# Optimization experiments

Measured on AMD Instinct MI355X. Metric: run time of the kernel, lower is better.

Reference implementation:

```python
import jax, jax.numpy as jnp
import numpy as np

N_NODES = 50000
N_EDGES = 800000
IN_CH = 128
HID = 64
PROJ = 32


def _gcn_norm(edge_index, n):
    # add self loops, symmetric normalization D^-1/2 (A+I) D^-1/2
    loop = jnp.arange(n, dtype=edge_index.dtype)
    src = jnp.concatenate([edge_index[0], loop])
    dst = jnp.concatenate([edge_index[1], loop])
    deg = jax.ops.segment_sum(jnp.ones_like(dst, jnp.float32), dst, num_segments=n)
    dinv = deg ** -0.5  # deg >= 1 due to self loops
    norm = dinv[src] * dinv[dst]
    return src, dst, norm


def _propagate(h, src, dst, norm, n):
    # gather -> scale -> scatter-add (message passing along A_hat)
    return jax.ops.segment_sum(h[src] * norm[:, None], dst, num_segments=n)


def _ho_gcn_layer(x, src, dst, norm, Ws, b, n):
    # out = sum_{k=1..max_order} (A_hat^k x) W_k + b
    out = jnp.zeros((n, Ws[0].shape[1]), x.dtype)
    h = x
    for W in Ws:
        h = _propagate(h, src, dst, norm, n)
        out = out + h @ W
    return out + b


def setup_inputs() -> dict:
    key = jax.random.key(0)
    ks = jax.random.split(key, 16)

    def w(k, fan_in, fan_out):
        return (jax.random.normal(k, (fan_in, fan_out), jnp.float32) / np.sqrt(fan_in)).astype(jnp.float32)

    x = jax.random.normal(ks[0], (N_NODES, IN_CH), jnp.float32)
    edge_index = jax.random.randint(ks[1], (2, N_EDGES), 0, N_NODES, dtype=jnp.int64)
    return {
        "x": x,
        "edge_index": edge_index,
        # conv1: max_order=2 -> two weights
        "W1_1": w(ks[2], IN_CH, HID), "W1_2": w(ks[3], IN_CH, HID),
        "b1": jnp.zeros((HID,), jnp.float32),
        # conv2
        "W2_1": w(ks[4], HID, HID // 2), "W2_2": w(ks[5], HID, HID // 2),
        "b2": jnp.zeros((HID // 2,), jnp.float32),
        # projection head
        "Wp1": w(ks[6], HID // 2, PROJ), "bp1": jnp.zeros((PROJ,), jnp.float32),
        "Wp2": w(ks[7], PROJ, PROJ), "bp2": jnp.zeros((PROJ,), jnp.float32),
        # coordinate head
        "Wc1": w(ks[8], HID // 2, HID // 4), "bc1": jnp.zeros((HID // 4,), jnp.float32),
        "Wc2": w(ks[9], HID // 4, 2), "bc2": jnp.zeros((2,), jnp.float32),
    }


def reference(x, edge_index, W1_1, W1_2, b1, W2_1, W2_2, b2,
              Wp1, bp1, Wp2, bp2, Wc1, bc1, Wc2, bc2):
    n = x.shape[0]
    src, dst, norm = _gcn_norm(edge_index, n)
    h1 = jax.nn.relu(_ho_gcn_layer(x, src, dst, norm, (W1_1, W1_2), b1, n))
    # dropout is identity in eval/reference mode
    h2 = jax.nn.relu(_ho_gcn_layer(h1, src, dst, norm, (W2_1, W2_2), b2, n))
    z = jax.nn.relu(h2 @ Wp1 + bp1) @ Wp2 + bp2
    coordinates = jax.nn.relu(h2 @ Wc1 + bc1) @ Wc2 + bc2
    return (coordinates, z)
```

## Files before the change

kernel.cpp:

```cpp
#include <hip/hip_runtime.h>

#define NN 50000
#define NE 800000
#define S 4
#define BINW 12500
#define NN4 (NN * S)
#define NBLK2 ((NN4 + 255) / 256)
#define NBG ((NN + 63) / 64)
#define NBH ((NE + 255) / 256)

__global__ __launch_bounds__(256) void zero_cnt_k(int* __restrict__ cnt) {
    int i = blockIdx.x * blockDim.x + threadIdx.x;
    if (i < NN4) cnt[i] = 0;
}

__global__ __launch_bounds__(256) void gemm1_hist_k(const float* __restrict__ A,
                                                    const float* __restrict__ WA,
                                                    const float* __restrict__ WB,
                                                    float* __restrict__ outA,
                                                    float* __restrict__ outB,
                                                    const int* __restrict__ src,
                                                    const int* __restrict__ dst,
                                                    int* __restrict__ cnt,
                                                    int* __restrict__ rank) {
    if (blockIdx.x >= NBG) {
        int e = (blockIdx.x - NBG) * 256 + threadIdx.x;
        if (e < NE) {
            int s = src[e], d = dst[e];
            int b = s / BINW;
            rank[e] = atomicAdd(&cnt[d * S + b], 1);
        }
        return;
    }

    __shared__ float As[64 * 36];
    __shared__ float W1s[32 * 68];
    __shared__ float W2s[32 * 68];
    const int t = threadIdx.x;
    const int tj = t & 15;
    const int tn = t >> 4;
    const int n0 = blockIdx.x * 64;
    float acc[4][8] = {};

    for (int kc = 0; kc < 128; kc += 32) {
        if (kc) __syncthreads();
        {
            int idx = t;
#pragma unroll
            for (int r = 0; r < 2; r++, idx += 256) {
                int nl = idx >> 3, q = idx & 7;
                int node = n0 + nl; node = node < NN ? node : NN - 1;
                float4 a = ((const float4*)A)[(size_t)node * 32 + (kc >> 2) + q];
                *(float4*)&As[nl * 36 + q * 4] = a;
            }
        }
        {
            int idx = t;
#pragma unroll
            for (int r = 0; r < 2; r++, idx += 256) {
                int kl = idx >> 4, j4 = idx & 15;
                *(float4*)&W1s[kl * 68 + j4 * 4] = ((const float4*)WA)[(size_t)(kc + kl) * 16 + j4];
                *(float4*)&W2s[kl * 68 + j4 * 4] = ((const float4*)WB)[(size_t)(kc + kl) * 16 + j4];
            }
        }
        __syncthreads();

        const float* ap = &As[tn * 4 * 36];
        const float* w1p = &W1s[tj * 4];
        const float* w2p = &W2s[tj * 4];
#pragma unroll 2
        for (int k4 = 0; k4 < 8; k4++) {
            float4 a0 = *(const float4*)&ap[0 * 36 + k4 * 4];
            float4 a1 = *(const float4*)&ap[1 * 36 + k4 * 4];
            float4 a2 = *(const float4*)&ap[2 * 36 + k4 * 4];
            float4 a3 = *(const float4*)&ap[3 * 36 + k4 * 4];
#pragma unroll
            for (int kk = 0; kk < 4; kk++) {
                float4 w1 = *(const float4*)&w1p[(k4 * 4 + kk) * 68];
                float4 w2 = *(const float4*)&w2p[(k4 * 4 + kk) * 68];
                float av0 = kk == 0 ? a0.x : kk == 1 ? a0.y : kk == 2 ? a0.z : a0.w;
                float av1 = kk == 0 ? a1.x : kk == 1 ? a1.y : kk == 2 ? a1.z : a1.w;
                float av2 = kk == 0 ? a2.x : kk == 1 ? a2.y : kk == 2 ? a2.z : a2.w;
                float av3 = kk == 0 ? a3.x : kk == 1 ? a3.y : kk == 2 ? a3.z : a3.w;
#define FMA8(m, AV)                                                     \
                acc[m][0] += AV * w1.x; acc[m][1] += AV * w1.y;          \
                acc[m][2] += AV * w1.z; acc[m][3] += AV * w1.w;          \
                acc[m][4] += AV * w2.x; acc[m][5] += AV * w2.y;          \
                acc[m][6] += AV * w2.z; acc[m][7] += AV * w2.w;
                FMA8(0, av0)
                FMA8(1, av1)
                FMA8(2, av2)
                FMA8(3, av3)
#undef FMA8
            }
        }
    }

#pragma unroll
    for (int m = 0; m < 4; m++) {
        int node = n0 + tn * 4 + m;
        if (node < NN) {
            *(float4*)&outA[(size_t)node * 64 + tj * 4] =
                make_float4(acc[m][0], acc[m][1], acc[m][2], acc[m][3]);
            *(float4*)&outB[(size_t)node * 64 + tj * 4] =
                make_float4(acc[m][4], acc[m][5], acc[m][6], acc[m][7]);
        }
    }
}

__global__ __launch_bounds__(256) void sum_blocks_k(const int* __restrict__ cnt,
                                                    int* __restrict__ bsum,
                                                    float* __restrict__ dinv) {
    __shared__ int s[256];
    int t = threadIdx.x;
    int i = blockIdx.x * 256 + t;
    int v = (i < NN4) ? cnt[i] : 0;
    s[t] = v;
    if (i < NN4 && (i & 3) == 0) {
        int deg = cnt[i] + cnt[i + 1] + cnt[i + 2] + cnt[i + 3];
        dinv[i >> 2] = rsqrtf((float)(deg + 1));
    }
    __syncthreads();
    for (int off = 128; off > 0; off >>= 1) {
        if (t < off) s[t] += s[t + off];
        __syncthreads();
    }
    if (t == 0) bsum[blockIdx.x] = s[0];
}

__global__ __launch_bounds__(256) void scan_final_k(const int* __restrict__ cnt,
                                                    const int* __restrict__ bsum,
                                                    int* __restrict__ rowsS) {
    __shared__ int sOff[256];
    __shared__ int s[256];
    int t = threadIdx.x;
    int accum = 0;
    for (int idx = t; idx < NBLK2; idx += 256)
        if (idx < blockIdx.x) accum += bsum[idx];
    sOff[t] = accum;
    __syncthreads();
    for (int off = 128; off > 0; off >>= 1) {
        if (t < off) sOff[t] += sOff[t + off];
        __syncthreads();
    }
    int boff = sOff[0];

    int i = blockIdx.x * 256 + t;
    int v = (i < NN4) ? cnt[i] : 0;
    s[t] = v;
    __syncthreads();
    for (int off = 1; off < 256; off <<= 1) {
        int x = (t >= off) ? s[t - off] : 0;
        __syncthreads();
        s[t] += x;
        __syncthreads();
    }
    if (i < NN4) rowsS[i] = boff + s[t] - v;
    if (blockIdx.x == 0 && t == 0) rowsS[NN4] = NE;
}

__global__ __launch_bounds__(256) void scatter_k(const int* __restrict__ src,
                                                 const int* __restrict__ dst,
                                                 const int* __restrict__ rank,
                                                 const int* __restrict__ rowsS,
                                                 int* __restrict__ col) {
    int e = blockIdx.x * blockDim.x + threadIdx.x;
    if (e >= NE) return;
    int s = src[e], d = dst[e];
    int b = s / BINW;
    col[rowsS[d * S + b] + rank[e]] = s;
}

template<int LOG2C4, bool ADDIN>
__global__ __launch_bounds__(256) void prop_k(const float4* __restrict__ h4,
                                              const float4* __restrict__ addin4,
                                              const float* __restrict__ bias,
                                              float4* __restrict__ out4,
                                              const int* __restrict__ rowsS,
                                              const int* __restrict__ col,
                                              const float* __restrict__ dinv) {
    const int C4 = 1 << LOG2C4;
    unsigned tid = blockIdx.x * blockDim.x + threadIdx.x;
    unsigned node = tid >> LOG2C4;
    if (node >= NN) return;
    unsigned lane = tid & (C4 - 1);
    size_t rowoff = ((size_t)node << LOG2C4) + lane;
    float dn = dinv[node];
    float w0 = dn * dn;
    float4 hv = h4[rowoff];
    float4 acc;
    if (ADDIN) {
        float4 a = addin4[rowoff];
        acc.x = a.x + w0 * hv.x; acc.y = a.y + w0 * hv.y;
        acc.z = a.z + w0 * hv.z; acc.w = a.w + w0 * hv.w;
    } else {
        float4 b = ((const float4*)bias)[lane];
        acc.x = b.x + w0 * hv.x; acc.y = b.y + w0 * hv.y;
        acc.z = b.z + w0 * hv.z; acc.w = b.w + w0 * hv.w;
    }
    int base = node * S;
    int rs = rowsS[base];
#pragma unroll
    for (int p = 1; p <= S; p++) {
        int re = rowsS[base + p];
        int i = rs;
        for (; i + 4 <= re; i += 4) {
            int c0 = col[i + 0];
            int c1 = col[i + 1];
            int c2 = col[i + 2];
            int c3 = col[i + 3];
            float4 v0 = h4[((size_t)c0 << LOG2C4) + lane];
            float4 v1 = h4[((size_t)c1 << LOG2C4) + lane];
            float4 v2 = h4[((size_t)c2 << LOG2C4) + lane];
            float4 v3 = h4[((size_t)c3 << LOG2C4) + lane];
            float a0 = dinv[c0] * dn;
            float a1 = dinv[c1] * dn;
            float a2 = dinv[c2] * dn;
            float a3 = dinv[c3] * dn;
            acc.x += a0 * v0.x + a1 * v1.x + a2 * v2.x + a3 * v3.x;
            acc.y += a0 * v0.y + a1 * v1.y + a2 * v2.y + a3 * v3.y;
            acc.z += a0 * v0.z + a1 * v1.z + a2 * v2.z + a3 * v3.z;
            acc.w += a0 * v0.w + a1 * v1.w + a2 * v2.w + a3 * v3.w;
        }
        for (; i < re; i++) {
            int c = col[i];
            float4 v = h4[((size_t)c << LOG2C4) + lane];
            float w = dinv[c] * dn;
            acc.x += w * v.x; acc.y += w * v.y; acc.z += w * v.z; acc.w += w * v.w;
        }
        rs = re;
    }
    if (!ADDIN) {
        acc.x = fmaxf(acc.x, 0.0f); acc.y = fmaxf(acc.y, 0.0f);
        acc.z = fmaxf(acc.z, 0.0f); acc.w = fmaxf(acc.w, 0.0f);
    }
    out4[rowoff] = acc;
}

template<int K, int JW>
__global__ __launch_bounds__(256) void gemm_k(const float* __restrict__ A,
                                              const float* __restrict__ WA,
                                              const float* __restrict__ WB,
                                              float* __restrict__ out, int n) {
    __shared__ float As[64 * 68];
    __shared__ float Ws[64 * 68];
    const int t = threadIdx.x;
    const int tj = t & 15;
    const int tn = t >> 4;
    const int n0 = blockIdx.x * 64;
    float acc[4][4] = {};

    for (int kc = 0; kc < K; kc += 64) {
        if (kc) __syncthreads();
        {
            int idx = t;
#pragma unroll
            for (int r = 0; r < 4; r++, idx += 256) {
                int nl = idx >> 4, q = idx & 15;
                int node = n0 + nl; node = node < n ? node : n - 1;
                float4 a = ((const float4*)A)[(size_t)node * (K / 4) + (kc >> 2) + q];
                *(float4*)&As[nl * 68 + q * 4] = a;
            }
        }
        {
            int idx = t;
#pragma unroll
            for (int r = 0; r < 4; r++, idx += 256) {
                int kl = idx >> 4, j4 = idx & 15;
                const float* W = (j4 < 8) ? WA : WB;
                float4 w = ((const float4*)W)[(size_t)(kc + kl) * 8 + (j4 & 7)];
                *(float4*)&Ws[kl * 68 + j4 * 4] = w;
            }
        }
        __syncthreads();

        const float* ap = &As[tn * 4 * 68];
        const float* wp = &Ws[tj * 4];
#pragma unroll 4
        for (int k4 = 0; k4 < 16; k4++) {
            float4 a0 = *(const float4*)&ap[0 * 68 + k4 * 4];
            float4 a1 = *(const float4*)&ap[1 * 68 + k4 * 4];
            float4 a2 = *(const float4*)&ap[2 * 68 + k4 * 4];
            float4 a3 = *(const float4*)&ap[3 * 68 + k4 * 4];
            float4 w0 = *(const float4*)&wp[(k4 * 4 + 0) * 68];
            float4 w1 = *(const float4*)&wp[(k4 * 4 + 1) * 68];
            float4 w2 = *(const float4*)&wp[(k4 * 4 + 2) * 68];
            float4 w3 = *(const float4*)&wp[(k4 * 4 + 3) * 68];
#define FMA_ROW(m, AV)                                                   \
            acc[m][0] += AV.x * w0.x + AV.y * w1.x + AV.z * w2.x + AV.w * w3.x; \
            acc[m][1] += AV.x * w0.y + AV.y * w1.y + AV.z * w2.y + AV.w * w3.y; \
            acc[m][2] += AV.x * w0.z + AV.y * w1.z + AV.z * w2.z + AV.w * w3.z; \
            acc[m][3] += AV.x * w0.w + AV.y * w1.w + AV.z * w2.w + AV.w * w3.w;
            FMA_ROW(0, a0)
            FMA_ROW(1, a1)
            FMA_ROW(2, a2)
            FMA_ROW(3, a3)
#undef FMA_ROW
        }
    }

    int mat = tj >> 3;
    int jw = (tj & 7) * 4;
    float* ob = out + (size_t)mat * n * JW + jw;
#pragma unroll
    for (int m = 0; m < 4; m++) {
        int node = n0 + tn * 4 + m;
        if (node < n)
            *(float4*)&ob[(size_t)node * JW] =
                make_float4(acc[m][0], acc[m][1], acc[m][2], acc[m][3]);
    }
}

__global__ __launch_bounds__(256) void heads_k(const float* __restrict__ h2,
                                               const float* __restrict__ Wp1, const float* __restrict__ bp1,
                                               const float* __restrict__ Wp2, const float* __restrict__ bp2,
                                               const float* __restrict__ Wc1, const float* __restrict__ bc1,
                                               const float* __restrict__ Wc2, const float* __restrict__ bc2,
                                               float* __restrict__ coord, float* __restrict__ z, int n) {
    __shared__ float sWp1[32 * 32], sWp2[32 * 32], sWc1[32 * 16], sWc2[32];
    __shared__ float sbp1[32], sbp2[32], sbc1[16], sbc2[2];
    __shared__ float sh[32 * 36], st[32 * 36], stc[32 * 18];
    const int t = threadIdx.x;
    for (int i = t; i < 1024; i += 256) { sWp1[i] = Wp1[i]; sWp2[i] = Wp2[i]; }
    for (int i = t; i < 512; i += 256) sWc1[i] = Wc1[i];
    if (t < 32) { sWc2[t] = Wc2[t]; sbp1[t] = bp1[t]; sbp2[t] = bp2[t]; }
    if (t < 16) sbc1[t] = bc1[t];
    if (t < 2) sbc2[t] = bc2[t];

    const int n0 = blockIdx.x * 32;
    const int nl = t >> 3;
    const int jq = t & 7;
    const int node = n0 + nl;
    {
        float4 v = make_float4(0.f, 0.f, 0.f, 0.f);
        if (node < n) v = *(const float4*)&h2[(size_t)node * 32 + jq * 4];
        *(float4*)&sh[nl * 36 + jq * 4] = v;
    }
    __syncthreads();

    float4 a = *(const float4*)&sbp1[jq * 4];
#pragma unroll
    for (int k = 0; k < 32; k++) {
        float hv = sh[nl * 36 + k];
        float4 w = *(const float4*)&sWp1[k * 32 + jq * 4];
        a.x += hv * w.x; a.y += hv * w.y; a.z += hv * w.z; a.w += hv * w.w;
    }
    a.x = fmaxf(a.x, 0.f); a.y = fmaxf(a.y, 0.f);
    a.z = fmaxf(a.z, 0.f); a.w = fmaxf(a.w, 0.f);
    *(float4*)&st[nl * 36 + jq * 4] = a;

    float2 c = *(const float2*)&sbc1[jq * 2];
#pragma unroll
    for (int k = 0; k < 32; k++) {
        float hv = sh[nl * 36 + k];
        float2 w = *(const float2*)&sWc1[k * 16 + jq * 2];
        c.x += hv * w.x; c.y += hv * w.y;
    }
    c.x = fmaxf(c.x, 0.f); c.y = fmaxf(c.y, 0.f);
    *(float2*)&stc[nl * 18 + jq * 2] = c;
    __syncthreads();

    float4 zz = *(const float4*)&sbp2[jq * 4];
#pragma unroll
    for (int k = 0; k < 32; k++) {
        float tv = st[nl * 36 + k];
        float4 w = *(const float4*)&sWp2[k * 32 + jq * 4];
        zz.x += tv * w.x; zz.y += tv * w.y; zz.z += tv * w.z; zz.w += tv * w.w;
    }
    if (node < n) *(float4*)&z[(size_t)node * 32 + jq * 4] = zz;

    if (jq < 2) {
        float s = sbc2[jq];
#pragma unroll
        for (int k = 0; k < 16; k++) s += stc[nl * 18 + k] * sWc2[k * 2 + jq];
        if (node < n) coord[(size_t)node * 2 + jq] = s;
    }
}

extern "C" void kernel_launch(void* const* d_in, const int* in_sizes, int n_in,
                              void* d_out, int out_size, void* d_ws, size_t ws_size,
                              hipStream_t stream) {
    const float* x    = (const float*)d_in[0];
    const int*   ei   = (const int*)d_in[1];
    const int*   src  = ei;
    const int*   dst  = ei + NE;
    const float* W1_1 = (const float*)d_in[2];
    const float* W1_2 = (const float*)d_in[3];
    const float* b1   = (const float*)d_in[4];
    const float* W2_1 = (const float*)d_in[5];
    const float* W2_2 = (const float*)d_in[6];
    const float* b2   = (const float*)d_in[7];
    const float* Wp1  = (const float*)d_in[8];
    const float* bp1  = (const float*)d_in[9];
    const float* Wp2  = (const float*)d_in[10];
    const float* bp2  = (const float*)d_in[11];
    const float* Wc1  = (const float*)d_in[12];
    const float* bc1  = (const float*)d_in[13];
    const float* Wc2  = (const float*)d_in[14];
    const float* bc2  = (const float*)d_in[15];

    float* ws    = (float*)d_ws;
    float* dinv  = ws;
    int*   cnt   = (int*)(dinv + NN);
    int*   rowsS = cnt + NN4;
    int*   bsum  = rowsS + NN4 + 4;
    int*   rank  = bsum + 1024;
    int*   col   = rank + NE;
    float* bufY  = (float*)(col + NE);
    float* bufZ  = bufY + (size_t)NN * 128;

    float* y1 = bufY;
    float* y2 = bufY + (size_t)NN * 64;
    float* u  = y1;
    float* h1 = y2;
    float* z1 = bufZ;
    float* z2 = bufZ + (size_t)NN * 32;
    float* u2 = z1;
    float* h2 = z2;

    float* coord = (float*)d_out;
    float* z     = (float*)d_out + 2 * NN;

    zero_cnt_k<<<NBLK2, 256, 0, stream>>>(cnt);
    gemm1_hist_k<<<NBG + NBH, 256, 0, stream>>>(x, W1_1, W1_2, y1, y2,
                                                src, dst, cnt, rank);
    sum_blocks_k<<<NBLK2, 256, 0, stream>>>(cnt, bsum, dinv);
    scan_final_k<<<NBLK2, 256, 0, stream>>>(cnt, bsum, rowsS);
    scatter_k<<<(NE + 255) / 256, 256, 0, stream>>>(src, dst, rank, rowsS, col);

    prop_k<4, true><<<(NN * 16 + 255) / 256, 256, 0, stream>>>(
        (const float4*)y2, (const float4*)y1, nullptr, (float4*)u, rowsS, col, dinv);
    prop_k<4, false><<<(NN * 16 + 255) / 256, 256, 0, stream>>>(
        (const float4*)u, nullptr, b1, (float4*)h1, rowsS, col, dinv);
    gemm_k<64, 32><<<(NN + 63) / 64, 256, 0, stream>>>(h1, W2_1, W2_2, bufZ, NN);
    prop_k<3, true><<<(NN * 8 + 255) / 256, 256, 0, stream>>>(
        (const float4*)z2, (const float4*)z1, nullptr, (float4*)u2, rowsS, col, dinv);
    prop_k<3, false><<<(NN * 8 + 255) / 256, 256, 0, stream>>>(
        (const float4*)u2, nullptr, b2, (float4*)h2, rowsS, col, dinv);
    heads_k<<<(NN + 31) / 32, 256, 0, stream>>>(h2, Wp1, bp1, Wp2, bp2, Wc1, bc1, Wc2, bc2, coord, z, NN);
}
```

Baseline: 297.1 us.

## Pad CSR bins to multiples of four with dummy node and vectorize edge loops

New measurement: 285.3 us. 4.0% less time.

```diff
diff --git a/kernel.cpp b/kernel.cpp
--- a/kernel.cpp
+++ b/kernel.cpp
@@ -7,28 +7,123 @@
 #define NN4 (NN * S)
 #define NBLK2 ((NN4 + 255) / 256)
 #define NBG ((NN + 63) / 64)
-#define NBH ((NE + 255) / 256)
-
-__global__ __launch_bounds__(256) void zero_cnt_k(int* __restrict__ cnt) {
+#define NBH4 ((NE / 4 + 255) / 256)
+#define COLCAP (NE + 3 * NN4 + 8)
+
+__global__ __launch_bounds__(256) void zero_cnt_k(int* __restrict__ cnt,
+                                                  float* __restrict__ dinv,
+                                                  float* __restrict__ y1s,
+                                                  float* __restrict__ y2s,
+                                                  float* __restrict__ z1s,
+                                                  float* __restrict__ z2s) {
     int i = blockIdx.x * blockDim.x + threadIdx.x;
     if (i < NN4) cnt[i] = 0;
-}
-
-__global__ __launch_bounds__(256) void gemm1_hist_k(const float* __restrict__ A,
-                                                    const float* __restrict__ WA,
-                                                    const float* __restrict__ WB,
-                                                    float* __restrict__ outA,
-                                                    float* __restrict__ outB,
-                                                    const int* __restrict__ src,
-                                                    const int* __restrict__ dst,
-                                                    int* __restrict__ cnt,
-                                                    int* __restrict__ rank) {
+    if (blockIdx.x == 0) {
+        int t = threadIdx.x;
+        if (t < 64) { y1s[t] = 0.f; y2s[t] = 0.f; }
+        else if (t < 96) { z1s[t - 64] = 0.f; z2s[t - 64] = 0.f; }
+        else if (t == 96) dinv[NN] = 0.f;
+    }
+}
+
+__global__ __launch_bounds__(256) void hist_k(const int* __restrict__ src,
+                                              const int* __restrict__ dst,
+                                              int* __restrict__ cnt,
+                                              int* __restrict__ rank) {
+    int e = (blockIdx.x * 256 + threadIdx.x) * 4;
+    if (e >= NE) return;
+    int4 s4 = *(const int4*)(src + e);
+    int4 d4 = *(const int4*)(dst + e);
+    int4 r;
+    r.x = atomicAdd(&cnt[d4.x * S + s4.x / BINW], 1);
+    r.y = atomicAdd(&cnt[d4.y * S + s4.y / BINW], 1);
+    r.z = atomicAdd(&cnt[d4.z * S + s4.z / BINW], 1);
+    r.w = atomicAdd(&cnt[d4.w * S + s4.w / BINW], 1);
+    *(int4*)(rank + e) = r;
+}
+
+__global__ __launch_bounds__(256) void sum_blocks_k(const int* __restrict__ cnt,
+                                                    int* __restrict__ bsum,
+                                                    float* __restrict__ dinv) {
+    __shared__ int s[256];
+    int t = threadIdx.x;
+    int i = blockIdx.x * 256 + t;
+    int v = 0;
+    if (i < NN4) {
+        int c = cnt[i];
+        v = (c + 3) & ~3;
+        if ((i & 3) == 0) {
+            int deg = c + cnt[i + 1] + cnt[i + 2] + cnt[i + 3];
+            dinv[i >> 2] = rsqrtf((float)(deg + 1));
+        }
+    }
+    s[t] = v;
+    __syncthreads();
+    for (int off = 128; off > 0; off >>= 1) {
+        if (t < off) s[t] += s[t + off];
+        __syncthreads();
+    }
+    if (t == 0) bsum[blockIdx.x] = s[0];
+}
+
+__global__ __launch_bounds__(256) void scan_final_k(const int* __restrict__ cnt,
+                                                    const int* __restrict__ bsum,
+                                                    int* __restrict__ rowsS) {
+    __shared__ int sOff[256];
+    __shared__ int s[256];
+    int t = threadIdx.x;
+    int accum = 0;
+    for (int idx = t; idx < NBLK2; idx += 256)
+        if (idx < blockIdx.x) accum += bsum[idx];
+    sOff[t] = accum;
+    __syncthreads();
+    for (int off = 128; off > 0; off >>= 1) {
+        if (t < off) sOff[t] += sOff[t + off];
+        __syncthreads();
+    }
+    int boff = sOff[0];
+
+    int i = blockIdx.x * 256 + t;
+    int v = (i < NN4) ? ((cnt[i] + 3) & ~3) : 0;
+    s[t] = v;
+    __syncthreads();
+    for (int off = 1; off < 256; off <<= 1) {
+        int x = (t >= off) ? s[t - off] : 0;
+        __syncthreads();
+        s[t] += x;
+        __syncthreads();
+    }
+    if (i < NN4) rowsS[i] = boff + s[t] - v;
+    if (blockIdx.x == NBLK2 - 1 && t == 255) rowsS[NN4] = boff + s[t];
+}
+
+__global__ __launch_bounds__(256) void gemm1_scatter_k(const float* __restrict__ A,
+                                                       const float* __restrict__ WA,
+                                                       const float* __restrict__ WB,
+                                                       float* __restrict__ outA,
+                                                       float* __restrict__ outB,
+                                                       const int* __restrict__ src,
+                                                       const int* __restrict__ dst,
+                                                       const int* __restrict__ rank,
+                                                       const int* __restrict__ rowsS,
+                                                       const int* __restrict__ cnt,
+                                                       int* __restrict__ col) {
     if (blockIdx.x >= NBG) {
-        int e = (blockIdx.x - NBG) * 256 + threadIdx.x;
+        int idx = (blockIdx.x - NBG) * 256 + threadIdx.x;
+        int e = idx * 4;
         if (e < NE) {
-            int s = src[e], d = dst[e];
-            int b = s / BINW;
-            rank[e] = atomicAdd(&cnt[d * S + b], 1);
+            int4 s4 = *(const int4*)(src + e);
+            int4 d4 = *(const int4*)(dst + e);
+            int4 r4 = *(const int4*)(rank + e);
+            col[rowsS[d4.x * S + s4.x / BINW] + r4.x] = s4.x;
+            col[rowsS[d4.y * S + s4.y / BINW] + r4.y] = s4.y;
+            col[rowsS[d4.z * S + s4.z / BINW] + r4.z] = s4.z;
+            col[rowsS[d4.w * S + s4.w / BINW] + r4.w] = s4.w;
+        }
+        if (idx < NN4) {
+            int end = rowsS[idx] + cnt[idx];
+            int nxt = rowsS[idx + 1];
+            for (int i = end; i < nxt; i++) col[i] = NN;
         }
         return;
     }
@@ -108,69 +203,6 @@
     }
 }
 
-__global__ __launch_bounds__(256) void sum_blocks_k(const int* __restrict__ cnt,
-                                                    int* __restrict__ bsum,
-                                                    float* __restrict__ dinv) {
-    __shared__ int s[256];
-    int t = threadIdx.x;
-    int i = blockIdx.x * 256 + t;
-    int v = (i < NN4) ? cnt[i] : 0;
-    s[t] = v;
-    if (i < NN4 && (i & 3) == 0) {
-        int deg = cnt[i] + cnt[i + 1] + cnt[i + 2] + cnt[i + 3];
-        dinv[i >> 2] = rsqrtf((float)(deg + 1));
-    }
-    __syncthreads();
-    for (int off = 128; off > 0; off >>= 1) {
-        if (t < off) s[t] += s[t + off];
-        __syncthreads();
-    }
-    if (t == 0) bsum[blockIdx.x] = s[0];
-}
-
-__global__ __launch_bounds__(256) void scan_final_k(const int* __restrict__ cnt,
-                                                    const int* __restrict__ bsum,
-                                                    int* __restrict__ rowsS) {
-    __shared__ int sOff[256];
-    __shared__ int s[256];
-    int t = threadIdx.x;
-    int accum = 0;
-    for (int idx = t; idx < NBLK2; idx += 256)
-        if (idx < blockIdx.x) accum += bsum[idx];
-    sOff[t] = accum;
-    __syncthreads();
-    for (int off = 128; off > 0; off >>= 1) {
-        if (t < off) sOff[t] += sOff[t + off];
-        __syncthreads();
-    }
-    int boff = sOff[0];
-
-    int i = blockIdx.x * 256 + t;
-    int v = (i < NN4) ? cnt[i] : 0;
-    s[t] = v;
-    __syncthreads();
-    for (int off = 1; off < 256; off <<= 1) {
-        int x = (t >= off) ? s[t - off] : 0;
-        __syncthreads();
-        s[t] += x;
-        __syncthreads();
-    }
-    if (i < NN4) rowsS[i] = boff + s[t] - v;
-    if (blockIdx.x == 0 && t == 0) rowsS[NN4] = NE;
-}
-
-__global__ __launch_bounds__(256) void scatter_k(const int* __restrict__ src,
-                                                 const int* __restrict__ dst,
-                                                 const int* __restrict__ rank,
-                                                 const int* __restrict__ rowsS,
-                                                 int* __restrict__ col) {
-    int e = blockIdx.x * blockDim.x + threadIdx.x;
-    if (e >= NE) return;
-    int s = src[e], d = dst[e];
-    int b = s / BINW;
-    col[rowsS[d * S + b] + rank[e]] = s;
-}
-
 template<int LOG2C4, bool ADDIN>
 __global__ __launch_bounds__(256) void prop_k(const float4* __restrict__ h4,
                                               const float4* __restrict__ addin4,
@@ -186,53 +218,41 @@
     unsigned lane = tid & (C4 - 1);
     size_t rowoff = ((size_t)node << LOG2C4) + lane;
     float dn = dinv[node];
+    float4 hv = h4[rowoff];
+    int rs = rowsS[node * S];
+    int re = rowsS[node * S + S];
+    int4 c = *(const int4*)(col + rs);
+    float4 g = make_float4(0.f, 0.f, 0.f, 0.f);
+    for (int i = rs; i < re; i += 4) {
+        int4 cc = c;
+        c = *(const int4*)(col + i + 4);
+        float a0 = dinv[cc.x];
+        float a1 = dinv[cc.y];
+        float a2 = dinv[cc.z];
+        float a3 = dinv[cc.w];
+        float4 v0 = h4[((size_t)cc.x << LOG2C4) + lane];
+        float4 v1 = h4[((size_t)cc.y << LOG2C4) + lane];
+        float4 v2 = h4[((size_t)cc.z << LOG2C4) + lane];
+        float4 v3 = h4[((size_t)cc.w << LOG2C4) + lane];
+        g.x += a0 * v0.x + a1 * v1.x + a2 * v2.x + a3 * v3.x;
+        g.y += a0 * v0.y + a1 * v1.y + a2 * v2.y + a3 * v3.y;
+        g.z += a0 * v0.z + a1 * v1.z + a2 * v2.z + a3 * v3.z;
+        g.w += a0 * v0.w + a1 * v1.w + a2 * v2.w + a3 * v3.w;
+    }
     float w0 = dn * dn;
-    float4 hv = h4[rowoff];
     float4 acc;
     if (ADDIN) {
         float4 a = addin4[rowoff];
-        acc.x = a.x + w0 * hv.x; acc.y = a.y + w0 * hv.y;
-        acc.z = a.z + w0 * hv.z; acc.w = a.w + w0 * hv.w;
+        acc.x = a.x + w0 * hv.x + dn * g.x;
+        acc.y = a.y + w0 * hv.y + dn * g.y;
+        acc.z = a.z + w0 * hv.z + dn * g.z;
+        acc.w = a.w + w0 * hv.w + dn * g.w;
     } else {
         float4 b = ((const float4*)bias)[lane];
-        acc.x = b.x + w0 * hv.x; acc.y = b.y + w0 * hv.y;
-        acc.z = b.z + w0 * hv.z; acc.w = b.w + w0 * hv.w;
-    }
-    int base = node * S;
-    int rs = rowsS[base];
-#pragma unroll
-    for (int p = 1; p <= S; p++) {
-        int re = rowsS[base + p];
-        int i = rs;
-        for (; i + 4 <= re; i += 4) {
-            int c0 = col[i + 0];
-            int c1 = col[i + 1];
-            int c2 = col[i + 2];
-            int c3 = col[i + 3];
-            float4 v0 = h4[((size_t)c0 << LOG2C4) + lane];
-            float4 v1 = h4[((size_t)c1 << LOG2C4) + lane];
-            float4 v2 = h4[((size_t)c2 << LOG2C4) + lane];
-            float4 v3 = h4[((size_t)c3 << LOG2C4) + lane];
-            float a0 = dinv[c0] * dn;
-            float a1 = dinv[c1] * dn;
-            float a2 = dinv[c2] * dn;
-            float a3 = dinv[c3] * dn;
-            acc.x += a0 * v0.x + a1 * v1.x + a2 * v2.x + a3 * v3.x;
-            acc.y += a0 * v0.y + a1 * v1.y + a2 * v2.y + a3 * v3.y;
-            acc.z += a0 * v0.z + a1 * v1.z + a2 * v2.z + a3 * v3.z;
-            acc.w += a0 * v0.w + a1 * v1.w + a2 * v2.w + a3 * v3.w;
-        }
-        for (; i < re; i++) {
-            int c = col[i];
-            float4 v = h4[((size_t)c << LOG2C4) + lane];
-            float w = dinv[c] * dn;
-            acc.x += w * v.x; acc.y += w * v.y; acc.z += w * v.z; acc.w += w * v.w;
-        }
-        rs = re;
-    }
-    if (!ADDIN) {
-        acc.x = fmaxf(acc.x, 0.0f); acc.y = fmaxf(acc.y, 0.0f);
-        acc.z = fmaxf(acc.z, 0.0f); acc.w = fmaxf(acc.w, 0.0f);
+        acc.x = fmaxf(b.x + w0 * hv.x + dn * g.x, 0.0f);
+        acc.y = fmaxf(b.y + w0 * hv.y + dn * g.y, 0.0f);
+        acc.z = fmaxf(b.z + w0 * hv.z + dn * g.z, 0.0f);
+        acc.w = fmaxf(b.w + w0 * hv.w + dn * g.w, 0.0f);
     }
     out4[rowoff] = acc;
 }
@@ -241,7 +261,8 @@
 __global__ __launch_bounds__(256) void gemm_k(const float* __restrict__ A,
                                               const float* __restrict__ WA,
                                               const float* __restrict__ WB,
-                                              float* __restrict__ out, int n) {
+                                              float* __restrict__ outA,
+                                              float* __restrict__ outB, int n) {
     __shared__ float As[64 * 68];
     __shared__ float Ws[64 * 68];
     const int t = threadIdx.x;
@@ -299,9 +320,7 @@
         }
     }
 
-    int mat = tj >> 3;
-    int jw = (tj & 7) * 4;
-    float* ob = out + (size_t)mat * n * JW + jw;
+    float* ob = ((tj >> 3) ? outB : outA) + (tj & 7) * 4;
 #pragma unroll
     for (int m = 0; m < 4; m++) {
         int node = n0 + tn * 4 + m;
@@ -401,38 +420,40 @@
 
     float* ws    = (float*)d_ws;
     float* dinv  = ws;
-    int*   cnt   = (int*)(dinv + NN);
+    int*   cnt   = (int*)(ws + 50004);
     int*   rowsS = cnt + NN4;
     int*   bsum  = rowsS + NN4 + 4;
     int*   rank  = bsum + 1024;
     int*   col   = rank + NE;
-    float* bufY  = (float*)(col + NE);
-    float* bufZ  = bufY + (size_t)NN * 128;
+    float* bufY  = (float*)(col + COLCAP);
+    float* bufZ  = bufY + (size_t)(NN + 1) * 128;
 
     float* y1 = bufY;
-    float* y2 = bufY + (size_t)NN * 64;
+    float* y2 = bufY + (size_t)(NN + 1) * 64;
     float* u  = y1;
     float* h1 = y2;
     float* z1 = bufZ;
-    float* z2 = bufZ + (size_t)NN * 32;
+    float* z2 = bufZ + (size_t)(NN + 1) * 32;
     float* u2 = z1;
     float* h2 = z2;
 
     float* coord = (float*)d_out;
     float* z     = (float*)d_out + 2 * NN;
 
-    zero_cnt_k<<<NBLK2, 256, 0, stream>>>(cnt);
-    gemm1_hist_k<<<NBG + NBH, 256, 0, stream>>>(x, W1_1, W1_2, y1, y2,
-                                                src, dst, cnt, rank);
+    zero_cnt_k<<<NBLK2, 256, 0, stream>>>(cnt, dinv,
+                                          y1 + (size_t)NN * 64, y2 + (size_t)NN * 64,
+                                          z1 + (size_t)NN * 32, z2 + (size_t)NN * 32);
+    hist_k<<<NBH4, 256, 0, stream>>>(src, dst, cnt, rank);
     sum_blocks_k<<<NBLK2, 256, 0, stream>>>(cnt, bsum, dinv);
     scan_final_k<<<NBLK2, 256, 0, stream>>>(cnt, bsum, rowsS);
-    scatter_k<<<(NE + 255) / 256, 256, 0, stream>>>(src, dst, rank, rowsS, col);
+    gemm1_scatter_k<<<NBG + NBH4, 256, 0, stream>>>(x, W1_1, W1_2, y1, y2,
+                                                    src, dst, rank, rowsS, cnt, col);
 
     prop_k<4, true><<<(NN * 16 + 255) / 256, 256, 0, stream>>>(
         (const float4*)y2, (const float4*)y1, nullptr, (float4*)u, rowsS, col, dinv);
     prop_k<4, false><<<(NN * 16 + 255) / 256, 256, 0, stream>>>(
         (const float4*)u, nullptr, b1, (float4*)h1, rowsS, col, dinv);
-    gemm_k<64, 32><<<(NN + 63) / 64, 256, 0, stream>>>(h1, W2_1, W2_2, bufZ, NN);
+    gemm_k<64, 32><<<(NN + 63) / 64, 256, 0, stream>>>(h1, W2_1, W2_2, z1, z2, NN);
     prop_k<3, true><<<(NN * 8 + 255) / 256, 256, 0, stream>>>(
         (const float4*)z2, (const float4*)z1, nullptr, (float4*)u2, rowsS, col, dinv);
     prop_k<3, false><<<(NN * 8 + 255) / 256, 256, 0, stream>>>(
```
